# Kernel optimization log

Hardware: AMD Instinct MI355X
Metric: run time of the kernel (lower is better)

Reference implementation:

```python
import jax, jax.numpy as jnp
import numpy as np

N = 100000
DIM = 128
E_A = 500000
E_D = 500000


def setup_inputs() -> dict:
    key = jax.random.key(0)
    ks = jax.random.split(key, 8)
    h = jax.random.normal(ks[0], (N, DIM), dtype=jnp.float32)
    a_idx = jax.random.randint(ks[1], (E_A, 3), 0, N, dtype=jnp.int64 if jax.config.jax_enable_x64 else jnp.int32)
    a_val = jax.random.uniform(ks[2], (E_A, 1), dtype=jnp.float32)
    d_idx = jax.random.randint(ks[3], (E_D, 4), 0, N, dtype=jnp.int64 if jax.config.jax_enable_x64 else jnp.int32)
    d_val = jax.random.uniform(ks[4], (E_D, 1), dtype=jnp.float32)
    # Linear weights stored as [in, out]; init ~ Kaiming-uniform-ish scale
    W_a = jax.random.normal(ks[5], (3 * DIM + 1, DIM), dtype=jnp.float32) * (1.0 / np.sqrt(3 * DIM + 1))
    b_a = jnp.zeros((DIM,), dtype=jnp.float32)
    W_d = jax.random.normal(ks[6], (4 * DIM + 1, DIM), dtype=jnp.float32) * (1.0 / np.sqrt(4 * DIM + 1))
    b_d = jnp.zeros((DIM,), dtype=jnp.float32)
    W_h = jax.random.normal(ks[7], (3 * DIM, DIM), dtype=jnp.float32) * (1.0 / np.sqrt(3 * DIM))
    b_h = jnp.zeros((DIM,), dtype=jnp.float32)
    return {"h": h, "a_idx": a_idx, "a_val": a_val, "d_idx": d_idx, "d_val": d_val,
            "W_a": W_a, "b_a": b_a, "W_d": W_d, "b_d": b_d, "W_h": W_h, "b_h": b_h}


def reference(h, a_idx, a_val, d_idx, d_val, W_a, b_a, W_d, b_d, W_h, b_h):
    n = h.shape[0]
    # angle messages: gather 3 node embeddings + scalar, Linear + SiLU, scatter to center node
    x_a = jnp.concatenate([h[a_idx[:, 0]], h[a_idx[:, 1]], h[a_idx[:, 2]], a_val], axis=-1)  # [E_a, 3d+1]
    m_ijk = jax.nn.silu(x_a @ W_a + b_a)  # [E_a, d]
    agg_a = jax.ops.segment_sum(m_ijk, a_idx[:, 1], num_segments=n)  # [N, d]
    # dihedral messages: gather 4 node embeddings + scalar
    x_d = jnp.concatenate([h[d_idx[:, 0]], h[d_idx[:, 1]], h[d_idx[:, 2]], h[d_idx[:, 3]], d_val], axis=-1)  # [E_d, 4d+1]
    m_ijkl = jax.nn.silu(x_d @ W_d + b_d)  # [E_d, d]
    agg_d = jax.ops.segment_sum(m_ijkl, d_idx[:, 1], num_segments=n)  # [N, d]
    # residual node update
    return h + jnp.concatenate([h, agg_a, agg_d], axis=-1) @ W_h + b_h
```

## Files before the change

kernel.cpp:

```cpp
#include <hip/hip_runtime.h>
#include <hip/hip_bf16.h>

#define DIM 128
#define LDS_STRIDE 136
#define SC_STRIDE 132

typedef __attribute__((ext_vector_type(8))) __bf16 bf16x8;
typedef __attribute__((ext_vector_type(4))) __bf16 bf16x4;
typedef __attribute__((ext_vector_type(2))) __bf16 bf16x2;
typedef __attribute__((ext_vector_type(4))) float f32x4;

__global__ __launch_bounds__(256) void prep_w(const float* __restrict__ W_a,
                                              const float* __restrict__ W_d,
                                              const float* __restrict__ W_h,
                                              __bf16* __restrict__ Wt)
{
    int idx = blockIdx.x * 256 + threadIdx.x;
    if (idx >= 10 * 16384) return;
    int t   = idx >> 14;
    int rem = idx & 16383;
    int c   = rem >> 7;
    int k   = rem & 127;
    const float* src;
    if (t < 3)      src = W_a + (size_t)t * 16384;
    else if (t < 7) src = W_d + (size_t)(t - 3) * 16384;
    else            src = W_h + (size_t)(t - 7) * 16384;
    Wt[(size_t)t * 16384 + c * 128 + k] = (__bf16)src[k * 128 + c];
}

__device__ __forceinline__ void stage_wt(const __bf16* __restrict__ Wtj,
                                         __bf16 (*sB)[LDS_STRIDE], int tid)
{
    for (int it = 0; it < 8; ++it) {
        int idx = tid + it * 256;
        int c  = idx >> 4;
        int k8 = (idx & 15) << 3;
        *(bf16x8*)&sB[c][k8] = *(const bf16x8*)(Wtj + c * 128 + k8);
    }
}

__device__ __forceinline__ void load_afrag_f32(const float* __restrict__ src,
                                               int row, int lk, int N, bf16x8 afrag[4])
{
    const float* rp = src + (size_t)row * DIM;
    #pragma unroll
    for (int ks = 0; ks < 4; ++ks) {
        float4 v0 = make_float4(0.f, 0.f, 0.f, 0.f), v1 = v0;
        if (row < N) {
            v0 = *(const float4*)(rp + ks * 32 + lk);
            v1 = *(const float4*)(rp + ks * 32 + lk + 4);
        }
        bf16x8 a;
        a[0] = (__bf16)v0.x; a[1] = (__bf16)v0.y; a[2] = (__bf16)v0.z; a[3] = (__bf16)v0.w;
        a[4] = (__bf16)v1.x; a[5] = (__bf16)v1.y; a[6] = (__bf16)v1.z; a[7] = (__bf16)v1.w;
        afrag[ks] = a;
    }
}

__device__ __forceinline__ void load_afrag_bf16(const __bf16* __restrict__ src,
                                                int row, int lk, int N, bf16x8 afrag[4])
{
    const __bf16* rp = src + (size_t)row * DIM;
    #pragma unroll
    for (int ks = 0; ks < 4; ++ks) {
        bf16x8 a = {};
        if (row < N) a = *(const bf16x8*)(rp + ks * 32 + lk);
        afrag[ks] = a;
    }
}

__global__ __launch_bounds__(256, 4) void proj(const float* __restrict__ src,
                                               const __bf16* __restrict__ Wt,
                                               __bf16* __restrict__ dst,
                                               int nj, int N)
{
    __shared__ __bf16 sB[128][LDS_STRIDE];
    float* sC = reinterpret_cast<float*>(sB);
    const int tid = threadIdx.x;
    const int node0 = blockIdx.x * 64;
    const int wave = tid >> 6, lane = tid & 63;
    const int lrow = lane & 15;
    const int lk   = (lane >> 4) * 8;
    const int arow = node0 + wave * 16 + lrow;

    bf16x8 afrag[4];
    load_afrag_f32(src, arow, lk, N, afrag);

    for (int j = 0; j < nj; ++j) {
        __syncthreads();
        stage_wt(Wt + (size_t)j * 16384, sB, tid);
        __syncthreads();

        f32x4 acc[8];
        #pragma unroll
        for (int ct = 0; ct < 8; ++ct) acc[ct] = (f32x4){0.f, 0.f, 0.f, 0.f};

        #pragma unroll
        for (int ks = 0; ks < 4; ++ks) {
            int k0 = ks * 32 + lk;
            #pragma unroll
            for (int ct = 0; ct < 8; ++ct) {
                bf16x8 b = *(const bf16x8*)&sB[ct * 16 + lrow][k0];
                acc[ct] = __builtin_amdgcn_mfma_f32_16x16x32_bf16(afrag[ks], b, acc[ct], 0, 0, 0);
            }
        }

        __syncthreads();
        {
            int rbase = wave * 16 + (lane >> 4) * 4;
            #pragma unroll
            for (int r = 0; r < 4; ++r)
                #pragma unroll
                for (int ct = 0; ct < 8; ++ct)
                    sC[(rbase + r) * SC_STRIDE + ct * 16 + lrow] = acc[ct][r];
        }
        __syncthreads();

        __bf16* dj = dst + (size_t)j * N * DIM;
        for (int it = 0; it < 8; ++it) {
            int idx = tid + it * 256;
            int row = idx >> 5;
            int c4  = (idx & 31) << 2;
            int grow = node0 + row;
            if (grow < N) {
                const float* sp = sC + row * SC_STRIDE + c4;
                bf16x4 o;
                o[0] = (__bf16)sp[0]; o[1] = (__bf16)sp[1];
                o[2] = (__bf16)sp[2]; o[3] = (__bf16)sp[3];
                *(bf16x4*)(dj + (size_t)grow * DIM + c4) = o;
            }
        }
    }
}

__global__ __launch_bounds__(256) void csr_count_both(const int* __restrict__ a_idx,
                                                      const int* __restrict__ d_idx,
                                                      int* __restrict__ offs,
                                                      int EA, int ED, int N)
{
    int e = blockIdx.x * 256 + threadIdx.x;
    if (e < EA) {
        atomicAdd(&offs[a_idx[3 * (size_t)e + 1]], 1);
    } else if (e < EA + ED) {
        int k = e - EA;
        atomicAdd(&offs[N + d_idx[4 * (size_t)k + 1]], 1);
    }
}

#define SCAN_CHUNK 1024

__global__ __launch_bounds__(256) void scan_s1(int* __restrict__ data,
                                               int* __restrict__ partials, int n)
{
    __shared__ int lds[256];
    const int t = threadIdx.x;
    const int base = blockIdx.x * SCAN_CHUNK + t * 4;
    int v[4];
    #pragma unroll
    for (int i = 0; i < 4; ++i) v[i] = (base + i < n) ? data[base + i] : 0;
    int tsum = v[0] + v[1] + v[2] + v[3];
    lds[t] = tsum; __syncthreads();
    for (int off = 1; off < 256; off <<= 1) {
        int x = (t >= off) ? lds[t - off] : 0;
        __syncthreads();
        lds[t] += x;
        __syncthreads();
    }
    if (t == 255) partials[blockIdx.x] = lds[255];
    int run = lds[t] - tsum;
    #pragma unroll
    for (int i = 0; i < 4; ++i) {
        int nv = run; run += v[i];
        if (base + i < n) data[base + i] = nv;
    }
}

__global__ __launch_bounds__(256) void scan_s2(int* __restrict__ partials, int nb)
{
    __shared__ int lds[256];
    const int t = threadIdx.x;
    int v = (t < nb) ? partials[t] : 0;
    lds[t] = v; __syncthreads();
    for (int off = 1; off < 256; off <<= 1) {
        int x = (t >= off) ? lds[t - off] : 0;
        __syncthreads();
        lds[t] += x;
        __syncthreads();
    }
    if (t < nb) partials[t] = lds[t] - v;
}

__global__ __launch_bounds__(256) void scan_s3(int* __restrict__ data,
                                               const int* __restrict__ partials, int n)
{
    const int add = partials[blockIdx.x];
    const int base = blockIdx.x * SCAN_CHUNK + threadIdx.x * 4;
    #pragma unroll
    for (int i = 0; i < 4; ++i)
        if (base + i < n) data[base + i] += add;
}

__global__ __launch_bounds__(256) void csr_fill_both(const int* __restrict__ a_idx,
                                                     const float* __restrict__ a_val,
                                                     const int* __restrict__ d_idx,
                                                     const float* __restrict__ d_val,
                                                     int* __restrict__ offs,
                                                     int4* __restrict__ recs,
                                                     int EA, int ED, int N)
{
    int e = blockIdx.x * 256 + threadIdx.x;
    if (e < EA) {
        int i0 = a_idx[3 * (size_t)e + 0];
        int i1 = a_idx[3 * (size_t)e + 1];
        int i2 = a_idx[3 * (size_t)e + 2];
        int slot = atomicAdd(&offs[i1], 1);
        recs[slot] = make_int4(i0 * 256, i2 * 256, __float_as_int(a_val[e]), 0);
    } else if (e < EA + ED) {
        int k = e - EA;
        int i0 = d_idx[4 * (size_t)k + 0];
        int i1 = d_idx[4 * (size_t)k + 1];
        int i2 = d_idx[4 * (size_t)k + 2];
        int i3 = d_idx[4 * (size_t)k + 3];
        int slot = atomicAdd(&offs[N + i1], 1);
        recs[slot] = make_int4(i0 * 256, i2 * 256, i3 * 256, __float_as_int(d_val[k]));
    }
}

__device__ __forceinline__ float silu(float x) { return x / (1.f + __expf(-x)); }

__global__ __launch_bounds__(256) void gather3(const __bf16* __restrict__ P,
                                               const float* __restrict__ wlast,
                                               const float* __restrict__ bias,
                                               const int* __restrict__ offs,
                                               const int4* __restrict__ recs,
                                               __bf16* __restrict__ agg, int N)
{
    const int tid = threadIdx.x;
    const int n = blockIdx.x * 16 + (tid >> 4);
    if (n >= N) return;
    const int gl = tid & 15;
    const int fb = gl * 16;
    const size_t NBb = (size_t)N * DIM * 2;
    const char* P0b = (const char*)P;
    const char* P1b = P0b + NBb;
    const char* P2b = P0b + 2 * NBb;
    int start = (n == 0) ? 0 : offs[n - 1];
    int end = offs[n];

    float wl[8], base[8];
    {
        const float* wp = wlast + gl * 8;
        const float* bp = bias + gl * 8;
        bf16x8 p1 = *(const bf16x8*)(P1b + (size_t)n * 256 + fb);
        #pragma unroll
        for (int c = 0; c < 8; ++c) { wl[c] = wp[c]; base[c] = (float)p1[c] + bp[c]; }
    }
    float a[8] = {0.f, 0.f, 0.f, 0.f, 0.f, 0.f, 0.f, 0.f};

    int s = start;
    for (; s + 1 < end; s += 2) {
        int4 rA = recs[s];
        int4 rB = recs[s + 1];
        bf16x8 A0 = *(const bf16x8*)(P0b + rA.x + fb);
        bf16x8 A2 = *(const bf16x8*)(P2b + rA.y + fb);
        bf16x8 B0 = *(const bf16x8*)(P0b + rB.x + fb);
        bf16x8 B2 = *(const bf16x8*)(P2b + rB.y + fb);
        float vA = __int_as_float(rA.z), vB = __int_as_float(rB.z);
        #pragma unroll
        for (int c = 0; c < 8; ++c) {
            a[c] += silu((float)A0[c] + (float)A2[c] + vA * wl[c] + base[c])
                  + silu((float)B0[c] + (float)B2[c] + vB * wl[c] + base[c]);
        }
    }
    if (s < end) {
        int4 rA = recs[s];
        bf16x8 A0 = *(const bf16x8*)(P0b + rA.x + fb);
        bf16x8 A2 = *(const bf16x8*)(P2b + rA.y + fb);
        float vA = __int_as_float(rA.z);
        #pragma unroll
        for (int c = 0; c < 8; ++c)
            a[c] += silu((float)A0[c] + (float)A2[c] + vA * wl[c] + base[c]);
    }
    bf16x8 o;
    #pragma unroll
    for (int c = 0; c < 8; ++c) o[c] = (__bf16)a[c];
    *(bf16x8*)(agg + (size_t)n * DIM + gl * 8) = o;
}

__global__ __launch_bounds__(256) void gather4(const __bf16* __restrict__ P,
                                               const float* __restrict__ wlast,
                                               const float* __restrict__ bias,
                                               const int* __restrict__ offs_d,
                                               const int4* __restrict__ recs,
                                               __bf16* __restrict__ agg, int N)
{
    const int tid = threadIdx.x;
    const int n = blockIdx.x * 16 + (tid >> 4);
    if (n >= N) return;
    const int gl = tid & 15;
    const int fb = gl * 16;
    const size_t NBb = (size_t)N * DIM * 2;
    const char* P0b = (const char*)P;
    const char* P1b = P0b + NBb;
    const char* P2b = P0b + 2 * NBb;
    const char* P3b = P0b + 3 * NBb;
    int start = offs_d[n - 1];
    int end = offs_d[n];

    float wl[8], base[8];
    {
        const float* wp = wlast + gl * 8;
        const float* bp = bias + gl * 8;
        bf16x8 p1 = *(const bf16x8*)(P1b + (size_t)n * 256 + fb);
        #pragma unroll
        for (int c = 0; c < 8; ++c) { wl[c] = wp[c]; base[c] = (float)p1[c] + bp[c]; }
    }
    float a[8] = {0.f, 0.f, 0.f, 0.f, 0.f, 0.f, 0.f, 0.f};

    int s = start;
    for (; s + 1 < end; s += 2) {
        int4 rA = recs[s];
        int4 rB = recs[s + 1];
        bf16x8 A0 = *(const bf16x8*)(P0b + rA.x + fb);
        bf16x8 A2 = *(const bf16x8*)(P2b + rA.y + fb);
        bf16x8 A3 = *(const bf16x8*)(P3b + rA.z + fb);
        bf16x8 B0 = *(const bf16x8*)(P0b + rB.x + fb);
        bf16x8 B2 = *(const bf16x8*)(P2b + rB.y + fb);
        bf16x8 B3 = *(const bf16x8*)(P3b + rB.z + fb);
        float vA = __int_as_float(rA.w), vB = __int_as_float(rB.w);
        #pragma unroll
        for (int c = 0; c < 8; ++c) {
            a[c] += silu((float)A0[c] + (float)A2[c] + (float)A3[c] + vA * wl[c] + base[c])
                  + silu((float)B0[c] + (float)B2[c] + (float)B3[c] + vB * wl[c] + base[c]);
        }
    }
    if (s < end) {
        int4 rA = recs[s];
        bf16x8 A0 = *(const bf16x8*)(P0b + rA.x + fb);
        bf16x8 A2 = *(const bf16x8*)(P2b + rA.y + fb);
        bf16x8 A3 = *(const bf16x8*)(P3b + rA.z + fb);
        float vA = __int_as_float(rA.w);
        #pragma unroll
        for (int c = 0; c < 8; ++c)
            a[c] += silu((float)A0[c] + (float)A2[c] + (float)A3[c] + vA * wl[c] + base[c]);
    }
    bf16x8 o;
    #pragma unroll
    for (int c = 0; c < 8; ++c) o[c] = (__bf16)a[c];
    *(bf16x8*)(agg + (size_t)n * DIM + gl * 8) = o;
}

__global__ __launch_bounds__(256, 4) void update_gemm(const float* __restrict__ srcf,
                                                      const __bf16* __restrict__ srcb,
                                                      const __bf16* __restrict__ Wt,
                                                      const float* __restrict__ bh,
                                                      const float* resid,
                                                      float* out, int nsrc, int N)
{
    __shared__ __bf16 sB[128][LDS_STRIDE];
    float* sC = reinterpret_cast<float*>(sB);
    const int tid = threadIdx.x;
    const int node0 = blockIdx.x * 64;
    const int wave = tid >> 6, lane = tid & 63;
    const int lrow = lane & 15;
    const int lk   = (lane >> 4) * 8;
    const int arow = node0 + wave * 16 + lrow;

    f32x4 acc[8];
    #pragma unroll
    for (int ct = 0; ct < 8; ++ct) acc[ct] = (f32x4){0.f, 0.f, 0.f, 0.f};

    for (int s = 0; s < nsrc; ++s) {
        __syncthreads();
        stage_wt(Wt + (size_t)s * 16384, sB, tid);

        bf16x8 afrag[4];
        if (nsrc == 2 && s == 0) load_afrag_f32(srcf, arow, lk, N, afrag);
        else                     load_afrag_bf16(srcb, arow, lk, N, afrag);
        __syncthreads();

        #pragma unroll
        for (int ks = 0; ks < 4; ++ks) {
            int k0 = ks * 32 + lk;
            #pragma unroll
            for (int ct = 0; ct < 8; ++ct) {
                bf16x8 b = *(const bf16x8*)&sB[ct * 16 + lrow][k0];
                acc[ct] = __builtin_amdgcn_mfma_f32_16x16x32_bf16(afrag[ks], b, acc[ct], 0, 0, 0);
            }
        }
    }

    __syncthreads();
    {
        int rbase = wave * 16 + (lane >> 4) * 4;
        #pragma unroll
        for (int r = 0; r < 4; ++r)
            #pragma unroll
            for (int ct = 0; ct < 8; ++ct)
                sC[(rbase + r) * SC_STRIDE + ct * 16 + lrow] = acc[ct][r];
    }
    __syncthreads();

    for (int it = 0; it < 8; ++it) {
        int idx = tid + it * 256;
        int row = idx >> 5;
        int c4  = (idx & 31) << 2;
        int grow = node0 + row;
        if (grow < N) {
            const float* sp = sC + row * SC_STRIDE + c4;
            float4 rv = *(const float4*)(resid + (size_t)grow * DIM + c4);
            float4 bv = bh ? *(const float4*)(bh + c4) : make_float4(0.f, 0.f, 0.f, 0.f);
            float4 ov;
            ov.x = rv.x + bv.x + sp[0];
            ov.y = rv.y + bv.y + sp[1];
            ov.z = rv.z + bv.z + sp[2];
            ov.w = rv.w + bv.w + sp[3];
            *(float4*)(out + (size_t)grow * DIM + c4) = ov;
        }
    }
}

static inline size_t align16(size_t x) { return (x + 15) & ~(size_t)15; }

extern "C" void kernel_launch(void* const* d_in, const int* in_sizes, int n_in,
                              void* d_out, int out_size, void* d_ws, size_t ws_size,
                              hipStream_t stream)
{
    const float* h     = (const float*)d_in[0];
    const int*   a_idx = (const int*)d_in[1];
    const float* a_val = (const float*)d_in[2];
    const int*   d_idx = (const int*)d_in[3];
    const float* d_val = (const float*)d_in[4];
    const float* W_a   = (const float*)d_in[5];
    const float* b_a   = (const float*)d_in[6];
    const float* W_d   = (const float*)d_in[7];
    const float* b_d   = (const float*)d_in[8];
    const float* W_h   = (const float*)d_in[9];
    const float* b_h   = (const float*)d_in[10];
    float* out = (float*)d_out;

    const int N  = in_sizes[0] / DIM;
    const int EA = in_sizes[2];
    const int ED = in_sizes[4];
    const size_t NB = (size_t)N * DIM;
    const int twoN = 2 * N;
    const int NBLK = (twoN + SCAN_CHUNK - 1) / SCAN_CHUNK;

    size_t off = 0;
    __bf16* P   = (__bf16*)((char*)d_ws + off); off = align16(off + 4 * NB * sizeof(__bf16));
    __bf16* agg = (__bf16*)((char*)d_ws + off); off = align16(off + NB * sizeof(__bf16));
    int* offs     = (int*)((char*)d_ws + off);  off = align16(off + (size_t)twoN * sizeof(int));
    int* partials = (int*)((char*)d_ws + off);  off = align16(off + 256 * sizeof(int));
    int4* recs    = (int4*)((char*)d_ws + off); off = align16(off + (size_t)(EA + ED) * sizeof(int4));
    __bf16* Wt  = (__bf16*)((char*)d_ws + off); off = align16(off + (size_t)10 * 16384 * sizeof(__bf16));
    if (ws_size < off) return;

    const int NT64 = (N + 63) / 64;
    const int GE = (EA + ED + 255) / 256;
    const int GN16 = (N + 15) / 16;

    prep_w<<<(10 * 16384 + 255) / 256, 256, 0, stream>>>(W_a, W_d, W_h, Wt);

    hipMemsetAsync(offs, 0, (size_t)twoN * sizeof(int), stream);
    csr_count_both<<<GE, 256, 0, stream>>>(a_idx, d_idx, offs, EA, ED, N);
    scan_s1<<<NBLK, 256, 0, stream>>>(offs, partials, twoN);
    scan_s2<<<1, 256, 0, stream>>>(partials, NBLK);
    scan_s3<<<NBLK, 256, 0, stream>>>(offs, partials, twoN);
    csr_fill_both<<<GE, 256, 0, stream>>>(a_idx, a_val, d_idx, d_val, offs, recs, EA, ED, N);

    proj<<<NT64, 256, 0, stream>>>(h, Wt, P, 3, N);
    gather3<<<GN16, 256, 0, stream>>>(P, W_a + 384 * DIM, b_a, offs, recs, agg, N);
    update_gemm<<<NT64, 256, 0, stream>>>(h, agg, Wt + (size_t)7 * 16384, b_h, h, out, 2, N);

    proj<<<NT64, 256, 0, stream>>>(h, Wt + (size_t)3 * 16384, P, 4, N);
    gather4<<<GN16, 256, 0, stream>>>(P, W_d + 512 * DIM, b_d, offs + N, recs, agg, N);
    update_gemm<<<NT64, 256, 0, stream>>>(nullptr, agg, Wt + (size_t)9 * 16384, nullptr, out, out, 1, N);
}
```

Baseline: 385.5 us.

## Split proj across grid y and use full wave per node in gathers

The projection kernel no longer loops over weight slices inside each block. Each slice becomes its own block along grid y, which gives 3x/4x more blocks and drops the per-iteration barriers. The gather kernels now assign a full 64-lane wave per destination node instead of 16 lanes. Each half-wave processes alternate edges with 8-byte loads, and a cross-half shuffle reduction combines the two halves. This raises memory-level parallelism for the irregular gathers, at the cost of re-reading h rows per slice and more threads idle on low-degree nodes.

```diff
diff --git a/kernel.cpp b/kernel.cpp
--- a/kernel.cpp
+++ b/kernel.cpp
@@ -72,63 +72,61 @@
 __global__ __launch_bounds__(256, 4) void proj(const float* __restrict__ src,
                                                const __bf16* __restrict__ Wt,
                                                __bf16* __restrict__ dst,
-                                               int nj, int N)
+                                               int N)
 {
     __shared__ __bf16 sB[128][LDS_STRIDE];
     float* sC = reinterpret_cast<float*>(sB);
     const int tid = threadIdx.x;
+    const int j = blockIdx.y;
     const int node0 = blockIdx.x * 64;
     const int wave = tid >> 6, lane = tid & 63;
     const int lrow = lane & 15;
     const int lk   = (lane >> 4) * 8;
     const int arow = node0 + wave * 16 + lrow;
 
+    stage_wt(Wt + (size_t)j * 16384, sB, tid);
+
     bf16x8 afrag[4];
     load_afrag_f32(src, arow, lk, N, afrag);
-
-    for (int j = 0; j < nj; ++j) {
-        __syncthreads();
-        stage_wt(Wt + (size_t)j * 16384, sB, tid);
-        __syncthreads();
-
-        f32x4 acc[8];
-        #pragma unroll
-        for (int ct = 0; ct < 8; ++ct) acc[ct] = (f32x4){0.f, 0.f, 0.f, 0.f};
-
-        #pragma unroll
-        for (int ks = 0; ks < 4; ++ks) {
-            int k0 = ks * 32 + lk;
+    __syncthreads();
+
+    f32x4 acc[8];
+    #pragma unroll
+    for (int ct = 0; ct < 8; ++ct) acc[ct] = (f32x4){0.f, 0.f, 0.f, 0.f};
+
+    #pragma unroll
+    for (int ks = 0; ks < 4; ++ks) {
+        int k0 = ks * 32 + lk;
+        #pragma unroll
+        for (int ct = 0; ct < 8; ++ct) {
+            bf16x8 b = *(const bf16x8*)&sB[ct * 16 + lrow][k0];
+            acc[ct] = __builtin_amdgcn_mfma_f32_16x16x32_bf16(afrag[ks], b, acc[ct], 0, 0, 0);
+        }
+    }
+
+    __syncthreads();
+    {
+        int rbase = wave * 16 + (lane >> 4) * 4;
+        #pragma unroll
+        for (int r = 0; r < 4; ++r)
             #pragma unroll
-            for (int ct = 0; ct < 8; ++ct) {
-                bf16x8 b = *(const bf16x8*)&sB[ct * 16 + lrow][k0];
-                acc[ct] = __builtin_amdgcn_mfma_f32_16x16x32_bf16(afrag[ks], b, acc[ct], 0, 0, 0);
-            }
-        }
-
-        __syncthreads();
-        {
-            int rbase = wave * 16 + (lane >> 4) * 4;
-            #pragma unroll
-            for (int r = 0; r < 4; ++r)
-                #pragma unroll
-                for (int ct = 0; ct < 8; ++ct)
-                    sC[(rbase + r) * SC_STRIDE + ct * 16 + lrow] = acc[ct][r];
-        }
-        __syncthreads();
-
-        __bf16* dj = dst + (size_t)j * N * DIM;
-        for (int it = 0; it < 8; ++it) {
-            int idx = tid + it * 256;
-            int row = idx >> 5;
-            int c4  = (idx & 31) << 2;
-            int grow = node0 + row;
-            if (grow < N) {
-                const float* sp = sC + row * SC_STRIDE + c4;
-                bf16x4 o;
-                o[0] = (__bf16)sp[0]; o[1] = (__bf16)sp[1];
-                o[2] = (__bf16)sp[2]; o[3] = (__bf16)sp[3];
-                *(bf16x4*)(dj + (size_t)grow * DIM + c4) = o;
-            }
+            for (int ct = 0; ct < 8; ++ct)
+                sC[(rbase + r) * SC_STRIDE + ct * 16 + lrow] = acc[ct][r];
+    }
+    __syncthreads();
+
+    __bf16* dj = dst + (size_t)j * N * DIM;
+    for (int it = 0; it < 8; ++it) {
+        int idx = tid + it * 256;
+        int row = idx >> 5;
+        int c4  = (idx & 31) << 2;
+        int grow = node0 + row;
+        if (grow < N) {
+            const float* sp = sC + row * SC_STRIDE + c4;
+            bf16x4 o;
+            o[0] = (__bf16)sp[0]; o[1] = (__bf16)sp[1];
+            o[2] = (__bf16)sp[2]; o[3] = (__bf16)sp[3];
+            *(bf16x4*)(dj + (size_t)grow * DIM + c4) = o;
         }
     }
 }
@@ -236,10 +234,13 @@
                                                __bf16* __restrict__ agg, int N)
 {
     const int tid = threadIdx.x;
-    const int n = blockIdx.x * 16 + (tid >> 4);
+    const int n = blockIdx.x * 4 + (tid >> 6);
     if (n >= N) return;
-    const int gl = tid & 15;
-    const int fb = gl * 16;
+    const int lane = tid & 63;
+    const int half = lane >> 5;
+    const int gl = lane & 31;
+    const int f  = gl * 4;
+    const int fb = gl * 8;
     const size_t NBb = (size_t)N * DIM * 2;
     const char* P0b = (const char*)P;
     const char* P1b = P0b + NBb;
@@ -247,44 +248,47 @@
     int start = (n == 0) ? 0 : offs[n - 1];
     int end = offs[n];
 
-    float wl[8], base[8];
-    {
-        const float* wp = wlast + gl * 8;
-        const float* bp = bias + gl * 8;
-        bf16x8 p1 = *(const bf16x8*)(P1b + (size_t)n * 256 + fb);
-        #pragma unroll
-        for (int c = 0; c < 8; ++c) { wl[c] = wp[c]; base[c] = (float)p1[c] + bp[c]; }
-    }
-    float a[8] = {0.f, 0.f, 0.f, 0.f, 0.f, 0.f, 0.f, 0.f};
-
+    float wl[4], base[4];
+    {
+        const float* wp = wlast + f;
+        const float* bp = bias + f;
+        bf16x4 p1 = *(const bf16x4*)(P1b + (size_t)n * 256 + fb);
+        #pragma unroll
+        for (int c = 0; c < 4; ++c) { wl[c] = wp[c]; base[c] = (float)p1[c] + bp[c]; }
+    }
+    float a[4] = {0.f, 0.f, 0.f, 0.f};
+
+    const int cnt = end - start;
+    const int npair = cnt >> 1;
     int s = start;
-    for (; s + 1 < end; s += 2) {
-        int4 rA = recs[s];
-        int4 rB = recs[s + 1];
-        bf16x8 A0 = *(const bf16x8*)(P0b + rA.x + fb);
-        bf16x8 A2 = *(const bf16x8*)(P2b + rA.y + fb);
-        bf16x8 B0 = *(const bf16x8*)(P0b + rB.x + fb);
-        bf16x8 B2 = *(const bf16x8*)(P2b + rB.y + fb);
-        float vA = __int_as_float(rA.z), vB = __int_as_float(rB.z);
-        #pragma unroll
-        for (int c = 0; c < 8; ++c) {
-            a[c] += silu((float)A0[c] + (float)A2[c] + vA * wl[c] + base[c])
-                  + silu((float)B0[c] + (float)B2[c] + vB * wl[c] + base[c]);
-        }
-    }
-    if (s < end) {
-        int4 rA = recs[s];
-        bf16x8 A0 = *(const bf16x8*)(P0b + rA.x + fb);
-        bf16x8 A2 = *(const bf16x8*)(P2b + rA.y + fb);
-        float vA = __int_as_float(rA.z);
-        #pragma unroll
-        for (int c = 0; c < 8; ++c)
-            a[c] += silu((float)A0[c] + (float)A2[c] + vA * wl[c] + base[c]);
-    }
-    bf16x8 o;
-    #pragma unroll
-    for (int c = 0; c < 8; ++c) o[c] = (__bf16)a[c];
-    *(bf16x8*)(agg + (size_t)n * DIM + gl * 8) = o;
+    for (int p = 0; p < npair; ++p, s += 2) {
+        int4 r = recs[s + half];
+        bf16x4 q0 = *(const bf16x4*)(P0b + r.x + fb);
+        bf16x4 q2 = *(const bf16x4*)(P2b + r.y + fb);
+        float v = __int_as_float(r.z);
+        #pragma unroll
+        for (int c = 0; c < 4; ++c)
+            a[c] += silu((float)q0[c] + (float)q2[c] + v * wl[c] + base[c]);
+    }
+    if (cnt & 1) {
+        int4 r = recs[end - 1];
+        bf16x4 q0 = *(const bf16x4*)(P0b + r.x + fb);
+        bf16x4 q2 = *(const bf16x4*)(P2b + r.y + fb);
+        float v = __int_as_float(r.z);
+        if (half == 0) {
+            #pragma unroll
+            for (int c = 0; c < 4; ++c)
+                a[c] += silu((float)q0[c] + (float)q2[c] + v * wl[c] + base[c]);
+        }
+    }
+    #pragma unroll
+    for (int c = 0; c < 4; ++c) a[c] += __shfl_xor(a[c], 32, 64);
+    if (half == 0) {
+        bf16x4 o;
+        #pragma unroll
+        for (int c = 0; c < 4; ++c) o[c] = (__bf16)a[c];
+        *(bf16x4*)(agg + (size_t)n * DIM + f) = o;
+    }
 }
 
 __global__ __launch_bounds__(256) void gather4(const __bf16* __restrict__ P,
@@ -295,10 +299,13 @@
                                                __bf16* __restrict__ agg, int N)
 {
     const int tid = threadIdx.x;
-    const int n = blockIdx.x * 16 + (tid >> 4);
+    const int n = blockIdx.x * 4 + (tid >> 6);
     if (n >= N) return;
-    const int gl = tid & 15;
-    const int fb = gl * 16;
+    const int lane = tid & 63;
+    const int half = lane >> 5;
+    const int gl = lane & 31;
+    const int f  = gl * 4;
+    const int fb = gl * 8;
     const size_t NBb = (size_t)N * DIM * 2;
     const char* P0b = (const char*)P;
     const char* P1b = P0b + NBb;
@@ -307,47 +314,49 @@
     int start = offs_d[n - 1];
     int end = offs_d[n];
 
-    float wl[8], base[8];
-    {
-        const float* wp = wlast + gl * 8;
-        const float* bp = bias + gl * 8;
-        bf16x8 p1 = *(const bf16x8*)(P1b + (size_t)n * 256 + fb);
-        #pragma unroll
-        for (int c = 0; c < 8; ++c) { wl[c] = wp[c]; base[c] = (float)p1[c] + bp[c]; }
-    }
-    float a[8] = {0.f, 0.f, 0.f, 0.f, 0.f, 0.f, 0.f, 0.f};
-
+    float wl[4], base[4];
+    {
+        const float* wp = wlast + f;
+        const float* bp = bias + f;
+        bf16x4 p1 = *(const bf16x4*)(P1b + (size_t)n * 256 + fb);
+        #pragma unroll
+        for (int c = 0; c < 4; ++c) { wl[c] = wp[c]; base[c] = (float)p1[c] + bp[c]; }
+    }
+    float a[4] = {0.f, 0.f, 0.f, 0.f};
+
+    const int cnt = end - start;
+    const int npair = cnt >> 1;
     int s = start;
-    for (; s + 1 < end; s += 2) {
-        int4 rA = recs[s];
-        int4 rB = recs[s + 1];
-        bf16x8 A0 = *(const bf16x8*)(P0b + rA.x + fb);
-        bf16x8 A2 = *(const bf16x8*)(P2b + rA.y + fb);
-        bf16x8 A3 = *(const bf16x8*)(P3b + rA.z + fb);
-        bf16x8 B0 = *(const bf16x8*)(P0b + rB.x + fb);
-        bf16x8 B2 = *(const bf16x8*)(P2b + rB.y + fb);
-        bf16x8 B3 = *(const bf16x8*)(P3b + rB.z + fb);
-        float vA = __int_as_float(rA.w), vB = __int_as_float(rB.w);
-        #pragma unroll
-        for (int c = 0; c < 8; ++c) {
-            a[c] += silu((float)A0[c] + (float)A2[c] + (float)A3[c] + vA * wl[c] + base[c])
-                  + silu((float)B0[c] + (float)B2[c] + (float)B3[c] + vB * wl[c] + base[c]);
-        }
-    }
-    if (s < end) {
-        int4 rA = recs[s];
-        bf16x8 A0 = *(const bf16x8*)(P0b + rA.x + fb);
-        bf16x8 A2 = *(const bf16x8*)(P2b + rA.y + fb);
-        bf16x8 A3 = *(const bf16x8*)(P3b + rA.z + fb);
-        float vA = __int_as_float(rA.w);
-        #pragma unroll
-        for (int c = 0; c < 8; ++c)
-            a[c] += silu((float)A0[c] + (float)A2[c] + (float)A3[c] + vA * wl[c] + base[c]);
-    }
-    bf16x8 o;
-    #pragma unroll
-    for (int c = 0; c < 8; ++c) o[c] = (__bf16)a[c];
-    *(bf16x8*)(agg + (size_t)n * DIM + gl * 8) = o;
+    for (int p = 0; p < npair; ++p, s += 2) {
+        int4 r = recs[s + half];
+        bf16x4 q0 = *(const bf16x4*)(P0b + r.x + fb);
+        bf16x4 q2 = *(const bf16x4*)(P2b + r.y + fb);
+        bf16x4 q3 = *(const bf16x4*)(P3b + r.z + fb);
+        float v = __int_as_float(r.w);
+        #pragma unroll
+        for (int c = 0; c < 4; ++c)
+            a[c] += silu((float)q0[c] + (float)q2[c] + (float)q3[c] + v * wl[c] + base[c]);
+    }
+    if (cnt & 1) {
+        int4 r = recs[end - 1];
+        bf16x4 q0 = *(const bf16x4*)(P0b + r.x + fb);
+        bf16x4 q2 = *(const bf16x4*)(P2b + r.y + fb);
+        bf16x4 q3 = *(const bf16x4*)(P3b + r.z + fb);
+        float v = __int_as_float(r.w);
+        if (half == 0) {
+            #pragma unroll
+            for (int c = 0; c < 4; ++c)
+                a[c] += silu((float)q0[c] + (float)q2[c] + (float)q3[c] + v * wl[c] + base[c]);
+        }
+    }
+    #pragma unroll
+    for (int c = 0; c < 4; ++c) a[c] += __shfl_xor(a[c], 32, 64);
+    if (half == 0) {
+        bf16x4 o;
+        #pragma unroll
+        for (int c = 0; c < 4; ++c) o[c] = (__bf16)a[c];
+        *(bf16x4*)(agg + (size_t)n * DIM + f) = o;
+    }
 }
 
 __global__ __launch_bounds__(256, 4) void update_gemm(const float* __restrict__ srcf,
@@ -457,7 +466,7 @@
 
     const int NT64 = (N + 63) / 64;
     const int GE = (EA + ED + 255) / 256;
-    const int GN16 = (N + 15) / 16;
+    const int GN4 = (N + 3) / 4;
 
     prep_w<<<(10 * 16384 + 255) / 256, 256, 0, stream>>>(W_a, W_d, W_h, Wt);
 
@@ -468,11 +477,17 @@
     scan_s3<<<NBLK, 256, 0, stream>>>(offs, partials, twoN);
     csr_fill_both<<<GE, 256, 0, stream>>>(a_idx, a_val, d_idx, d_val, offs, recs, EA, ED, N);
 
-    proj<<<NT64, 256, 0, stream>>>(h, Wt, P, 3, N);
-    gather3<<<GN16, 256, 0, stream>>>(P, W_a + 384 * DIM, b_a, offs, recs, agg, N);
+    {
+        dim3 g(NT64, 3);
+        proj<<<g, 256, 0, stream>>>(h, Wt, P, N);
+    }
+    gather3<<<GN4, 256, 0, stream>>>(P, W_a + 384 * DIM, b_a, offs, recs, agg, N);
     update_gemm<<<NT64, 256, 0, stream>>>(h, agg, Wt + (size_t)7 * 16384, b_h, h, out, 2, N);
 
-    proj<<<NT64, 256, 0, stream>>>(h, Wt + (size_t)3 * 16384, P, 4, N);
-    gather4<<<GN16, 256, 0, stream>>>(P, W_d + 512 * DIM, b_d, offs + N, recs, agg, N);
+    {
+        dim3 g(NT64, 4);
+        proj<<<g, 256, 0, stream>>>(h, Wt + (size_t)3 * 16384, P, N);
+    }
+    gather4<<<GN4, 256, 0, stream>>>(P, W_d + 512 * DIM, b_d, offs + N, recs, agg, N);
     update_gemm<<<NT64, 256, 0, stream>>>(nullptr, agg, Wt + (size_t)9 * 16384, nullptr, out, out, 1, N);
 }
```

Measured after the change: 385.9 us. No clear change (+0.1%).
